# Performance work log

Measured on AMD Instinct MI355X. Metric: run time of the kernel, lower is better.

## Reference

```python
import jax, jax.numpy as jnp
import numpy as np

KH = KW = 3  # kernel_size

def _extract_patches(x):
    # x: [B, C, H, W] -> patches [B, C, Ho, Wo, KH*KW], same ordering as nn.Unfold
    B, C, H, W = x.shape
    Ho, Wo = H - KH + 1, W - KW + 1
    slices = [x[:, :, i:i + Ho, j:j + Wo] for i in range(KH) for j in range(KW)]
    return jnp.stack(slices, axis=-1)

def setup_inputs() -> dict:
    key = jax.random.key(0)
    k1, k2 = jax.random.split(key)
    x = jax.random.normal(k1, (16, 64, 128, 128), dtype=jnp.float32)
    W = jax.random.normal(k2, (8, KH * KW), dtype=jnp.float32) * (1.0 / np.sqrt(KH * KW))
    return {"x": x, "W": W}

def reference(x, W):
    # per-patch: out = Linear(SiLU(patch)) for each of n_convs kernels and each channel
    B, C, H, Wd = x.shape
    Ho, Wo = H - KH + 1, Wd - KW + 1
    patches = _extract_patches(x)                      # [B, C, Ho, Wo, 9]
    act = jax.nn.silu(patches)
    # out channel ordering: kern + channel * n_convs -> [B, C, K, Ho, Wo]
    out = jnp.einsum('bchwj,kj->bckhw', act, W)
    return out.reshape(B, C * W.shape[0], Ho, Wo)
```

## Files before the change

kernel.cpp:

```cpp
#include <hip/hip_runtime.h>

#define B_   16
#define C_   64
#define H_   128
#define W_   128
#define HO   126
#define WO   126
#define NK   8
#define ROWS 42
#define INR  44

__global__ __launch_bounds__(512) void conv_silu_kernel(
    const float* __restrict__ x, const float* __restrict__ Wt,
    float* __restrict__ out)
{
    __shared__ float s[INR][W_];

    const int band = blockIdx.x;
    const int c    = blockIdx.y;
    const int b    = blockIdx.z;
    const int tid  = threadIdx.x;
    const int ho0  = band * ROWS;

    {
        const float4* xv =
            (const float4*)(x + ((size_t)(b * C_ + c) * H_ + ho0) * W_);
#pragma unroll
        for (int i = 0; i < 3; ++i) {
            const int f = tid + i * 512;
            if (f < INR * (W_ / 4)) {
                const float4 v = xv[f];
                const int row = f >> 5;
                const int col = (f & 31) << 2;
                float4 sv;
                sv.x = v.x * __builtin_amdgcn_rcpf(1.0f + __expf(-v.x));
                sv.y = v.y * __builtin_amdgcn_rcpf(1.0f + __expf(-v.y));
                sv.z = v.z * __builtin_amdgcn_rcpf(1.0f + __expf(-v.z));
                sv.w = v.w * __builtin_amdgcn_rcpf(1.0f + __expf(-v.w));
                *(float4*)&s[row][col] = sv;
            }
        }
    }
    __syncthreads();

    const int l  = tid & 63;
    const int ws = __builtin_amdgcn_readfirstlane((int)(threadIdx.x >> 6));

    float w9[9];
#pragma unroll
    for (int j = 0; j < 9; ++j) w9[j] = Wt[ws * 9 + j];

    float* op = out + ((size_t)((b * C_ + c) * NK + ws) * HO + ho0) * WO;

    float tA[3][3], tB[3][3];
#pragma unroll
    for (int j = 0; j < 3; ++j) {
#pragma unroll
        for (int d = 0; d < 3; ++d) {
            tA[j][d] = s[j][l + d];
            tB[j][d] = s[j][(64 + l + d) & 127];
        }
    }

#pragma unroll
    for (int r = 0; r < ROWS; ++r) {
        float accA = 0.f, accB = 0.f;
#pragma unroll
        for (int j = 0; j < 3; ++j) {
#pragma unroll
            for (int d = 0; d < 3; ++d) {
                const float ww = w9[j * 3 + d];
                accA += ww * tA[j][d];
                accB += ww * tB[j][d];
            }
        }
        op[r * WO + l] = accA;
        if (l < 62) op[r * WO + 64 + l] = accB;

        if (r < ROWS - 1) {
#pragma unroll
            for (int j = 0; j < 2; ++j) {
#pragma unroll
                for (int d = 0; d < 3; ++d) {
                    tA[j][d] = tA[j + 1][d];
                    tB[j][d] = tB[j + 1][d];
                }
            }
#pragma unroll
            for (int d = 0; d < 3; ++d) {
                tA[2][d] = s[r + 3][l + d];
                tB[2][d] = s[r + 3][(64 + l + d) & 127];
            }
        }
    }
}

extern "C" void kernel_launch(void* const* d_in, const int* in_sizes, int n_in,
                              void* d_out, int out_size, void* d_ws, size_t ws_size,
                              hipStream_t stream) {
    const float* x  = (const float*)d_in[0];
    const float* Wt = (const float*)d_in[1];
    float* out = (float*)d_out;

    dim3 grid(3, C_, B_);
    conv_silu_kernel<<<grid, 512, 0, stream>>>(x, Wt, out);
}
```

Baseline: 124.9 us.

## Split row bands finer and compute two kernels per wave with 256-thread blocks

Each block now covers 14 output rows instead of 42, so the grid grows from 3 to 9 bands per channel. Blocks shrink to 256 threads, and each wave computes two of the eight output kernels from the same loaded patch registers. The aim is more, smaller blocks for better occupancy and load balance across CUs, plus reuse of each shared-memory read across two weights. The cost is more halo rows reloaded, with SiLU recomputed on them (16 input rows per 14 output rows versus 44 per 42).

Measured after the change: 129.9 us. 4.0% more time.

```diff
diff --git a/kernel.cpp b/kernel.cpp
--- a/kernel.cpp
+++ b/kernel.cpp
@@ -7,10 +7,10 @@
 #define HO   126
 #define WO   126
 #define NK   8
-#define ROWS 42
-#define INR  44
+#define ROWS 14
+#define INR  16
 
-__global__ __launch_bounds__(512) void conv_silu_kernel(
+__global__ __launch_bounds__(256, 8) void conv_silu_kernel(
     const float* __restrict__ x, const float* __restrict__ Wt,
     float* __restrict__ out)
 {
@@ -26,19 +26,17 @@
         const float4* xv =
             (const float4*)(x + ((size_t)(b * C_ + c) * H_ + ho0) * W_);
 #pragma unroll
-        for (int i = 0; i < 3; ++i) {
-            const int f = tid + i * 512;
-            if (f < INR * (W_ / 4)) {
-                const float4 v = xv[f];
-                const int row = f >> 5;
-                const int col = (f & 31) << 2;
-                float4 sv;
-                sv.x = v.x * __builtin_amdgcn_rcpf(1.0f + __expf(-v.x));
-                sv.y = v.y * __builtin_amdgcn_rcpf(1.0f + __expf(-v.y));
-                sv.z = v.z * __builtin_amdgcn_rcpf(1.0f + __expf(-v.z));
-                sv.w = v.w * __builtin_amdgcn_rcpf(1.0f + __expf(-v.w));
-                *(float4*)&s[row][col] = sv;
-            }
+        for (int i = 0; i < 2; ++i) {
+            const int f   = tid + i * 256;
+            const float4 v = xv[f];
+            const int row = f >> 5;
+            const int col = (f & 31) << 2;
+            float4 sv;
+            sv.x = v.x * __builtin_amdgcn_rcpf(1.0f + __expf(-v.x));
+            sv.y = v.y * __builtin_amdgcn_rcpf(1.0f + __expf(-v.y));
+            sv.z = v.z * __builtin_amdgcn_rcpf(1.0f + __expf(-v.z));
+            sv.w = v.w * __builtin_amdgcn_rcpf(1.0f + __expf(-v.w));
+            *(float4*)&s[row][col] = sv;
         }
     }
     __syncthreads();
@@ -46,11 +44,15 @@
     const int l  = tid & 63;
     const int ws = __builtin_amdgcn_readfirstlane((int)(threadIdx.x >> 6));
 
-    float w9[9];
+    float w0[9], w1[9];
 #pragma unroll
-    for (int j = 0; j < 9; ++j) w9[j] = Wt[ws * 9 + j];
+    for (int j = 0; j < 9; ++j) {
+        w0[j] = Wt[(2 * ws    ) * 9 + j];
+        w1[j] = Wt[(2 * ws + 1) * 9 + j];
+    }
 
-    float* op = out + ((size_t)((b * C_ + c) * NK + ws) * HO + ho0) * WO;
+    float* opA = out + ((size_t)((b * C_ + c) * NK + 2 * ws) * HO + ho0) * WO;
+    float* opB = opA + (size_t)HO * WO;
 
     float tA[3][3], tB[3][3];
 #pragma unroll
@@ -64,18 +66,25 @@
 
 #pragma unroll
     for (int r = 0; r < ROWS; ++r) {
-        float accA = 0.f, accB = 0.f;
+        float a0 = 0.f, a1 = 0.f, b0 = 0.f, b1 = 0.f;
 #pragma unroll
         for (int j = 0; j < 3; ++j) {
 #pragma unroll
             for (int d = 0; d < 3; ++d) {
-                const float ww = w9[j * 3 + d];
-                accA += ww * tA[j][d];
-                accB += ww * tB[j][d];
+                const float q0 = w0[j * 3 + d];
+                const float q1 = w1[j * 3 + d];
+                a0 += q0 * tA[j][d];
+                a1 += q1 * tA[j][d];
+                b0 += q0 * tB[j][d];
+                b1 += q1 * tB[j][d];
             }
         }
-        op[r * WO + l] = accA;
-        if (l < 62) op[r * WO + 64 + l] = accB;
+        opA[r * WO + l] = a0;
+        opB[r * WO + l] = a1;
+        if (l < 62) {
+            opA[r * WO + 64 + l] = b0;
+            opB[r * WO + 64 + l] = b1;
+        }
 
         if (r < ROWS - 1) {
 #pragma unroll
@@ -102,6 +111,6 @@
     const float* Wt = (const float*)d_in[1];
     float* out = (float*)d_out;
 
-    dim3 grid(3, C_, B_);
-    conv_silu_kernel<<<grid, 512, 0, stream>>>(x, Wt, out);
+    dim3 grid(9, C_, B_);
+    conv_silu_kernel<<<grid, 256, 0, stream>>>(x, Wt, out);
 }
```
